# Kernel tuning notes

Measured on AMD Instinct MI355X. Metric: run time of the kernel, lower is better.

Reference implementation:

```python
import math
import jax, jax.numpy as jnp
import numpy as np

B, W, C = 2, 2048, 1024
N, K = 16, 64  # heads, head dim (C // N)


def setup_inputs() -> dict:
    key = jax.random.key(0)
    ks = jax.random.split(key, 6)
    return {
        "in_sequence_bwc": jax.random.normal(ks[0], (B, W, C), dtype=jnp.float32),
        "W_proj": jax.random.normal(ks[1], (C, C), dtype=jnp.float32) * (1.0 / math.sqrt(C)),
        "b_proj": jax.random.normal(ks[2], (C,), dtype=jnp.float32) * 0.01,
        "generators_1nwk": jax.random.normal(ks[3], (1, N, W, K), dtype=jnp.float32),
        "W_mix": jax.random.normal(ks[4], (C, C), dtype=jnp.float32) * (1.0 / math.sqrt(C)),
        "b_mix": jax.random.normal(ks[5], (C,), dtype=jnp.float32) * 0.01,
    }


def reference(in_sequence_bwc, W_proj, b_proj, generators_1nwk, W_mix, b_mix):
    b, w, c = in_sequence_bwc.shape
    # shared projection (torch Linear: x @ W.T + b)
    p_bwc = in_sequence_bwc @ W_proj.T + b_proj
    p_bnwk = p_bwc.reshape(b, w, N, K).transpose(0, 2, 1, 3)  # [b, n, w, k]
    g_nwk = generators_1nwk[0, :, :w, :]  # [n, w, k]
    # data-dependent metric generator: p^T @ G -> [b, n, k, k]
    m_bnkk = jnp.einsum("bnwk,nwl->bnkl", p_bnwk, g_nwk)
    tril_kk = jnp.tril(jnp.ones((K, K), dtype=in_sequence_bwc.dtype))
    m_bnkk = m_bnkk * tril_kk  # lower-triangular mask on k x k
    m_bnkk = m_bnkk @ jnp.swapaxes(m_bnkk, -1, -2)  # PSD metric M M^T
    # bilinear scores: P @ M @ P^T, scaled
    pm_bnwk = jnp.einsum("bnwk,bnkl->bnwl", p_bnwk, m_bnkk)
    scores_bnww = jnp.einsum("bnwk,bnvk->bnwv", pm_bnwk, p_bnwk) / math.sqrt(K)
    causal = jnp.tril(jnp.ones((w, w), dtype=bool))
    scores_bnww = jnp.where(causal, scores_bnww, -jnp.inf)
    attn_bnww = jax.nn.softmax(scores_bnww, axis=-1)
    nudged_bnwk = attn_bnww @ p_bnwk
    nudged_bwc = nudged_bnwk.transpose(0, 2, 1, 3).reshape(b, w, c)
    return nudged_bwc @ W_mix.T + b_mix
```

## Files before the change

### kernel.cpp

```cpp
#include <hip/hip_runtime.h>
#include <math.h>

#define B_  2
#define W_  2048
#define C_  1024
#define NH_ 16
#define KD_ 64

__device__ __forceinline__ int sw(int r, int c) {
    return (r << 6) + ((((c >> 2) ^ ((r >> 2) & 7)) << 2) | (c & 3));
}

__device__ __forceinline__ void stage64s(const float* __restrict__ src,
                                         float* dst, int tid) {
#pragma unroll
    for (int q = 0; q < 4; ++q) {
        int idx = tid + (q << 8);
        int r   = idx >> 4;
        int c   = (idx & 15) << 2;
        *(float4*)&dst[sw(r, c)] = *(const float4*)(src + (idx << 2));
    }
}

__device__ __forceinline__ void stage64(const float* __restrict__ src,
                                        float (*dst)[68], int tid) {
#pragma unroll
    for (int q = 0; q < 4; ++q) {
        int idx = tid + (q << 8);
        int e   = idx << 2;
        int r   = e >> 6;
        int c   = e & 63;
        *(float4*)&dst[r][c] = *(const float4*)(src + e);
    }
}

template<int OUT_P_LAYOUT>
__global__ __launch_bounds__(256, 2)
void gemm_nt(const float* __restrict__ A, const float* __restrict__ Bw,
             const float* __restrict__ bias, float* __restrict__ Cout)
{
    __shared__ float As[16][68];
    __shared__ float Bs[16][68];
    const int tid = threadIdx.x;
    const int tx  = tid & 15, ty = tid >> 4;
    const int m0  = blockIdx.x << 6;
    const int n0  = blockIdx.y << 6;
    const int lrow = tid >> 2;
    const int lkq  = (tid & 3) << 2;
    const float* Ap = A  + (size_t)(m0 + lrow) * C_ + lkq;
    const float* Bp = Bw + (size_t)(n0 + lrow) * C_ + lkq;

    float acc[4][4] = {};
    for (int k0 = 0; k0 < C_; k0 += 16) {
        float4 av = *(const float4*)(Ap + k0);
        float4 bv = *(const float4*)(Bp + k0);
        __syncthreads();
        As[lkq+0][lrow] = av.x; As[lkq+1][lrow] = av.y;
        As[lkq+2][lrow] = av.z; As[lkq+3][lrow] = av.w;
        Bs[lkq+0][lrow] = bv.x; Bs[lkq+1][lrow] = bv.y;
        Bs[lkq+2][lrow] = bv.z; Bs[lkq+3][lrow] = bv.w;
        __syncthreads();
#pragma unroll
        for (int kk = 0; kk < 16; ++kk) {
            float4 a4 = *(const float4*)&As[kk][ty << 2];
            float4 b4 = *(const float4*)&Bs[kk][tx << 2];
            float am[4] = {a4.x, a4.y, a4.z, a4.w};
            float bm[4] = {b4.x, b4.y, b4.z, b4.w};
#pragma unroll
            for (int i = 0; i < 4; ++i)
#pragma unroll
                for (int j = 0; j < 4; ++j)
                    acc[i][j] = fmaf(am[i], bm[j], acc[i][j]);
        }
    }

    const int gc = n0 + (tx << 2);
    float4 bb = *(const float4*)&bias[gc];
#pragma unroll
    for (int i = 0; i < 4; ++i) {
        int gm = m0 + (ty << 2) + i;
        float4 o;
        o.x = acc[i][0] + bb.x;
        o.y = acc[i][1] + bb.y;
        o.z = acc[i][2] + bb.z;
        o.w = acc[i][3] + bb.w;
        if (OUT_P_LAYOUT) {
            int b = gm >> 11;
            int w = gm & 2047;
            int n = gc >> 6;
            int k = gc & 63;
            *(float4*)(Cout + (((size_t)(b * NH_ + n) * W_ + w) * KD_ + k)) = o;
        } else {
            *(float4*)(Cout + (size_t)gm * C_ + gc) = o;
        }
    }
}

__global__ __launch_bounds__(256, 2)
void metric_part(const float* __restrict__ p, const float* __restrict__ g,
                 float* __restrict__ part)
{
    __shared__ float Ps[32][68];
    __shared__ float Gs[32][68];
    const int ch  = blockIdx.x;
    const int bn  = blockIdx.y;
    const int n   = bn & (NH_ - 1);
    const int tid = threadIdx.x;
    const int tx  = tid & 15, ty = tid >> 4;
    const float* pb = p + (size_t)bn * W_ * KD_ + (size_t)(ch << 8) * KD_;
    const float* gb = g + (size_t)n  * W_ * KD_ + (size_t)(ch << 8) * KD_;

    float acc[4][4] = {};
    for (int w0 = 0; w0 < 256; w0 += 32) {
        __syncthreads();
#pragma unroll
        for (int q = 0; q < 2; ++q) {
            int idx = tid + (q << 8);
            int e   = idx << 2;
            int r   = e >> 6;
            int c   = e & 63;
            *(float4*)&Ps[r][c] = *(const float4*)(pb + (size_t)(w0 + r) * KD_ + c);
            *(float4*)&Gs[r][c] = *(const float4*)(gb + (size_t)(w0 + r) * KD_ + c);
        }
        __syncthreads();
#pragma unroll 8
        for (int w = 0; w < 32; ++w) {
            float4 a4 = *(const float4*)&Ps[w][ty << 2];
            float4 b4 = *(const float4*)&Gs[w][tx << 2];
            float am[4] = {a4.x, a4.y, a4.z, a4.w};
            float bm[4] = {b4.x, b4.y, b4.z, b4.w};
#pragma unroll
            for (int i = 0; i < 4; ++i)
#pragma unroll
                for (int j = 0; j < 4; ++j)
                    acc[i][j] = fmaf(am[i], bm[j], acc[i][j]);
        }
    }

    float* ob = part + (size_t)(bn * 8 + ch) * KD_ * KD_;
#pragma unroll
    for (int i = 0; i < 4; ++i) {
        float4 o; o.x = acc[i][0]; o.y = acc[i][1]; o.z = acc[i][2]; o.w = acc[i][3];
        *(float4*)(ob + ((ty << 2) + i) * KD_ + (tx << 2)) = o;
    }
}

__global__ __launch_bounds__(256, 2)
void metric_reduce(const float* __restrict__ part, float* __restrict__ m2)
{
    __shared__ float M1s[64][68];
    const int bn  = blockIdx.x;
    const int tid = threadIdx.x;
    const int tx  = tid & 15, ty = tid >> 4;
    const float* pb = part + (size_t)bn * 8 * KD_ * KD_;

#pragma unroll
    for (int v = 0; v < 4; ++v) {
        int f = tid + (v << 8);
        int e = f << 2;
        float4 s = *(const float4*)(pb + e);
#pragma unroll
        for (int c = 1; c < 8; ++c) {
            float4 t = *(const float4*)(pb + c * 4096 + e);
            s.x += t.x; s.y += t.y; s.z += t.z; s.w += t.w;
        }
        int k = e >> 6, l = e & 63;
        if (l + 0 > k) s.x = 0.f;
        if (l + 1 > k) s.y = 0.f;
        if (l + 2 > k) s.z = 0.f;
        if (l + 3 > k) s.w = 0.f;
        *(float4*)&M1s[k][l] = s;
    }
    __syncthreads();

    float a2[4][4] = {};
#pragma unroll
    for (int jq = 0; jq < 64; jq += 4) {
        float4 av[4], bv[4];
#pragma unroll
        for (int i = 0; i < 4; ++i) av[i] = *(const float4*)&M1s[(ty << 2) + i][jq];
#pragma unroll
        for (int j = 0; j < 4; ++j) bv[j] = *(const float4*)&M1s[(tx << 2) + j][jq];
#pragma unroll
        for (int i = 0; i < 4; ++i)
#pragma unroll
            for (int j = 0; j < 4; ++j)
                a2[i][j] += av[i].x * bv[j].x + av[i].y * bv[j].y +
                            av[i].z * bv[j].z + av[i].w * bv[j].w;
    }

    float* ob = m2 + (size_t)bn * KD_ * KD_;
#pragma unroll
    for (int i = 0; i < 4; ++i) {
        float4 o; o.x = a2[i][0]; o.y = a2[i][1]; o.z = a2[i][2]; o.w = a2[i][3];
        *(float4*)(ob + ((ty << 2) + i) * KD_ + (tx << 2)) = o;
    }
}

__global__ __launch_bounds__(256, 2)
void qgen_k(const float* __restrict__ p, const float* __restrict__ m2,
            float* __restrict__ qout)
{
    __shared__ float Pt[64][68];
    __shared__ float Ms[64][68];
    const int bn  = blockIdx.y;
    const int w0  = blockIdx.x << 6;
    const int tid = threadIdx.x;
    const int tx  = tid & 15, ty = tid >> 4;
    const float* pb = p  + (size_t)bn * W_ * KD_ + (size_t)w0 * KD_;
    const float* mb = m2 + (size_t)bn * KD_ * KD_;

    stage64(pb, Pt, tid);
    stage64(mb, Ms, tid);
    __syncthreads();

    float acc[4][4] = {};
#pragma unroll
    for (int kq = 0; kq < 64; kq += 4) {
        float4 av[4];
        float  bm[4][4];
#pragma unroll
        for (int i = 0; i < 4; ++i) av[i] = *(const float4*)&Pt[(ty << 2) + i][kq];
#pragma unroll
        for (int kk = 0; kk < 4; ++kk) {
            float4 t = *(const float4*)&Ms[kq + kk][tx << 2];
            bm[kk][0] = t.x; bm[kk][1] = t.y; bm[kk][2] = t.z; bm[kk][3] = t.w;
        }
#pragma unroll
        for (int i = 0; i < 4; ++i) {
            float am[4] = {av[i].x, av[i].y, av[i].z, av[i].w};
#pragma unroll
            for (int j = 0; j < 4; ++j)
                acc[i][j] = fmaf(am[0], bm[0][j],
                            fmaf(am[1], bm[1][j],
                            fmaf(am[2], bm[2][j],
                            fmaf(am[3], bm[3][j], acc[i][j]))));
        }
    }

    float* ob = qout + (size_t)bn * W_ * KD_ + (size_t)w0 * KD_;
#pragma unroll
    for (int i = 0; i < 4; ++i) {
        float4 o;
        o.x = acc[i][0] * 0.125f; o.y = acc[i][1] * 0.125f;
        o.z = acc[i][2] * 0.125f; o.w = acc[i][3] * 0.125f;
        *(float4*)(ob + ((ty << 2) + i) * KD_ + (tx << 2)) = o;
    }
}

__global__ __launch_bounds__(256, 2)
void attn_k(const float* __restrict__ qg, const float* __restrict__ p,
            float* __restrict__ nud)
{
    __shared__ float Qs[4096];
    __shared__ float Ks[4096];
    __shared__ float Es[4096];
    const int bid = blockIdx.x;
    const int bn  = bid & 31;
    const int qt  = 31 - (bid >> 5);
    const int b   = bn >> 4, n = bn & 15;
    const int tid = threadIdx.x;
    const int tx  = tid & 15, ty = tid >> 4;
    const float* qb = qg + (size_t)bn * W_ * KD_ + (size_t)(qt << 6) * KD_;
    const float* kb = p  + (size_t)bn * W_ * KD_;

    stage64s(qb, Qs, tid);

    float acc[4][4] = {};
    float mi[4], li[4];
#pragma unroll
    for (int i = 0; i < 4; ++i) { mi[i] = -INFINITY; li[i] = 0.f; }

    for (int j0 = 0; j0 <= qt; ++j0) {
        __syncthreads();
        stage64s(kb + (size_t)(j0 << 6) * KD_, Ks, tid);
        __syncthreads();

        float s[4][4] = {};
#pragma unroll
        for (int kq = 0; kq < 64; kq += 4) {
            float4 av[4], bv[4];
#pragma unroll
            for (int i = 0; i < 4; ++i) av[i] = *(const float4*)&Qs[sw((ty << 2) + i, kq)];
#pragma unroll
            for (int j = 0; j < 4; ++j) bv[j] = *(const float4*)&Ks[sw((tx << 2) + j, kq)];
#pragma unroll
            for (int i = 0; i < 4; ++i)
#pragma unroll
                for (int j = 0; j < 4; ++j)
                    s[i][j] = fmaf(av[i].x, bv[j].x,
                              fmaf(av[i].y, bv[j].y,
                              fmaf(av[i].z, bv[j].z,
                              fmaf(av[i].w, bv[j].w, s[i][j]))));
        }

        if (j0 == qt) {
#pragma unroll
            for (int i = 0; i < 4; ++i)
#pragma unroll
                for (int j = 0; j < 4; ++j)
                    if (((tx << 2) + j) > ((ty << 2) + i)) s[i][j] = -INFINITY;
        }

        float mnew[4], al[4];
#pragma unroll
        for (int i = 0; i < 4; ++i) {
            float rm = fmaxf(fmaxf(s[i][0], s[i][1]), fmaxf(s[i][2], s[i][3]));
            rm = fmaxf(rm, __shfl_xor(rm, 1, 16));
            rm = fmaxf(rm, __shfl_xor(rm, 2, 16));
            rm = fmaxf(rm, __shfl_xor(rm, 4, 16));
            rm = fmaxf(rm, __shfl_xor(rm, 8, 16));
            mnew[i] = fmaxf(mi[i], rm);
        }
#pragma unroll
        for (int i = 0; i < 4; ++i) {
#pragma unroll
            for (int j = 0; j < 4; ++j) s[i][j] = __expf(s[i][j] - mnew[i]);
            float rs = s[i][0] + s[i][1] + s[i][2] + s[i][3];
            rs += __shfl_xor(rs, 1, 16);
            rs += __shfl_xor(rs, 2, 16);
            rs += __shfl_xor(rs, 4, 16);
            rs += __shfl_xor(rs, 8, 16);
            al[i] = __expf(mi[i] - mnew[i]);
            li[i] = li[i] * al[i] + rs;
            mi[i] = mnew[i];
        }
#pragma unroll
        for (int i = 0; i < 4; ++i) {
            float4 e; e.x = s[i][0]; e.y = s[i][1]; e.z = s[i][2]; e.w = s[i][3];
            *(float4*)&Es[sw((ty << 2) + i, tx << 2)] = e;
#pragma unroll
            for (int j = 0; j < 4; ++j) acc[i][j] *= al[i];
        }
        __syncthreads();

#pragma unroll
        for (int jq = 0; jq < 64; jq += 4) {
            float4 av[4];
            float  vm[4][4];
#pragma unroll
            for (int i = 0; i < 4; ++i) av[i] = *(const float4*)&Es[sw((ty << 2) + i, jq)];
#pragma unroll
            for (int kk = 0; kk < 4; ++kk) {
                float4 t = *(const float4*)&Ks[sw(jq + kk, tx << 2)];
                vm[kk][0] = t.x; vm[kk][1] = t.y; vm[kk][2] = t.z; vm[kk][3] = t.w;
            }
#pragma unroll
            for (int i = 0; i < 4; ++i) {
                float am[4] = {av[i].x, av[i].y, av[i].z, av[i].w};
#pragma unroll
                for (int c = 0; c < 4; ++c)
                    acc[i][c] = fmaf(am[0], vm[0][c],
                                fmaf(am[1], vm[1][c],
                                fmaf(am[2], vm[2][c],
                                fmaf(am[3], vm[3][c], acc[i][c]))));
            }
        }
    }

    const int wrow = qt << 6;
#pragma unroll
    for (int i = 0; i < 4; ++i) {
        float inv = 1.f / li[i];
        float4 o;
        o.x = acc[i][0] * inv; o.y = acc[i][1] * inv;
        o.z = acc[i][2] * inv; o.w = acc[i][3] * inv;
        size_t row = (size_t)(b * W_ + wrow + (ty << 2) + i);
        *(float4*)(nud + row * C_ + (n << 6) + (tx << 2)) = o;
    }
}

extern "C" void kernel_launch(void* const* d_in, const int* in_sizes, int n_in,
                              void* d_out, int out_size, void* d_ws, size_t ws_size,
                              hipStream_t stream)
{
    (void)in_sizes; (void)n_in; (void)out_size; (void)ws_size;
    const float* X  = (const float*)d_in[0];
    const float* Wp = (const float*)d_in[1];
    const float* bp = (const float*)d_in[2];
    const float* G  = (const float*)d_in[3];
    const float* Wm = (const float*)d_in[4];
    const float* bm = (const float*)d_in[5];
    float* out = (float*)d_out;
    float* ws  = (float*)d_ws;

    float* Pbuf = ws;
    float* Qbuf = ws + 4194304;
    float* M2   = ws + 8388608;
    float* Nud  = ws + 8519680;
    float* Part = Qbuf;

    dim3 blk(256);
    gemm_nt<1>   <<<dim3(64, 16), blk, 0, stream>>>(X, Wp, bp, Pbuf);
    metric_part  <<<dim3(8, 32),  blk, 0, stream>>>(Pbuf, G, Part);
    metric_reduce<<<dim3(32),     blk, 0, stream>>>(Part, M2);
    qgen_k       <<<dim3(32, 32), blk, 0, stream>>>(Pbuf, M2, Qbuf);
    attn_k       <<<dim3(1024),   blk, 0, stream>>>(Qbuf, Pbuf, Nud);
    gemm_nt<0>   <<<dim3(64, 16), blk, 0, stream>>>(Nud, Wm, bm, out);
}
```

Before: 855.5 us.

## Read Q and K tiles directly from global memory in attention kernel

Removes the shared-memory staging of the Q and K/V tiles in the attention kernel and loads them straight from global memory (relying on L1/L2 caching), keeping only the probability tile in LDS. This drops two barriers per key tile and cuts LDS use, which allows raising the launch-bounds occupancy target from 2 to 4 blocks per CU. The block-to-query-tile mapping is also changed so blocks past the first 512 walk query tiles in ascending order. The risk is many redundant, poorly coalesced global loads, since each thread reads rows strided by 64 floats and the tiles are re-read per thread group instead of once per block.

```diff
diff --git a/kernel.cpp b/kernel.cpp
--- a/kernel.cpp
+++ b/kernel.cpp
@@ -9,17 +9,6 @@
 
 __device__ __forceinline__ int sw(int r, int c) {
     return (r << 6) + ((((c >> 2) ^ ((r >> 2) & 7)) << 2) | (c & 3));
-}
-
-__device__ __forceinline__ void stage64s(const float* __restrict__ src,
-                                         float* dst, int tid) {
-#pragma unroll
-    for (int q = 0; q < 4; ++q) {
-        int idx = tid + (q << 8);
-        int r   = idx >> 4;
-        int c   = (idx & 15) << 2;
-        *(float4*)&dst[sw(r, c)] = *(const float4*)(src + (idx << 2));
-    }
 }
 
 __device__ __forceinline__ void stage64(const float* __restrict__ src,
@@ -248,42 +237,41 @@
     }
 }
 
-__global__ __launch_bounds__(256, 2)
+__global__ __launch_bounds__(256, 4)
 void attn_k(const float* __restrict__ qg, const float* __restrict__ p,
             float* __restrict__ nud)
 {
-    __shared__ float Qs[4096];
-    __shared__ float Ks[4096];
     __shared__ float Es[4096];
     const int bid = blockIdx.x;
     const int bn  = bid & 31;
-    const int qt  = 31 - (bid >> 5);
+    const int qt  = (bid < 512) ? (31 - (bid >> 5)) : ((bid - 512) >> 5);
     const int b   = bn >> 4, n = bn & 15;
     const int tid = threadIdx.x;
     const int tx  = tid & 15, ty = tid >> 4;
     const float* qb = qg + (size_t)bn * W_ * KD_ + (size_t)(qt << 6) * KD_;
     const float* kb = p  + (size_t)bn * W_ * KD_;
 
-    stage64s(qb, Qs, tid);
-
     float acc[4][4] = {};
     float mi[4], li[4];
 #pragma unroll
     for (int i = 0; i < 4; ++i) { mi[i] = -INFINITY; li[i] = 0.f; }
 
+    const float* qv = qb;
+
     for (int j0 = 0; j0 <= qt; ++j0) {
-        __syncthreads();
-        stage64s(kb + (size_t)(j0 << 6) * KD_, Ks, tid);
-        __syncthreads();
+        asm volatile("" : "+v"(qv));
+        const float* kt = kb + (size_t)(j0 << 6) * KD_;
 
         float s[4][4] = {};
 #pragma unroll
-        for (int kq = 0; kq < 64; kq += 4) {
+        for (int kq = 0; kq < 16; ++kq) {
             float4 av[4], bv[4];
 #pragma unroll
-            for (int i = 0; i < 4; ++i) av[i] = *(const float4*)&Qs[sw((ty << 2) + i, kq)];
-#pragma unroll
-            for (int j = 0; j < 4; ++j) bv[j] = *(const float4*)&Ks[sw((tx << 2) + j, kq)];
+            for (int i = 0; i < 4; ++i)
+                av[i] = *(const float4*)(qv + ((ty << 2) + i) * KD_ + (kq << 2));
+#pragma unroll
+            for (int j = 0; j < 4; ++j)
+                bv[j] = *(const float4*)(kt + ((tx << 2) + j) * KD_ + (kq << 2));
 #pragma unroll
             for (int i = 0; i < 4; ++i)
 #pragma unroll
@@ -325,6 +313,8 @@
             li[i] = li[i] * al[i] + rs;
             mi[i] = mnew[i];
         }
+
+        __syncthreads();
 #pragma unroll
         for (int i = 0; i < 4; ++i) {
             float4 e; e.x = s[i][0]; e.y = s[i][1]; e.z = s[i][2]; e.w = s[i][3];
@@ -342,7 +332,7 @@
             for (int i = 0; i < 4; ++i) av[i] = *(const float4*)&Es[sw((ty << 2) + i, jq)];
 #pragma unroll
             for (int kk = 0; kk < 4; ++kk) {
-                float4 t = *(const float4*)&Ks[sw(jq + kk, tx << 2)];
+                float4 t = *(const float4*)(kt + (size_t)(jq + kk) * KD_ + (tx << 2));
                 vm[kk][0] = t.x; vm[kk][1] = t.y; vm[kk][2] = t.z; vm[kk][3] = t.w;
             }
 #pragma unroll
```

New measurement: 1.069 ms. 1.25x slower.

## Double-buffer K tiles with register prefetch in attention kernel

Applied to the files above, without the earlier changes.

The attention kernel now keeps two shared-memory K buffers. It loads the next K tile into registers while computing scores for the current one, then writes it to the alternate buffer before the PV pass. This overlaps global-load latency with compute and removes one barrier per iteration. It also reorders block-to-query-tile assignment so the second half of blocks walks light tiles in ascending order, at the cost of more LDS and register pressure.

```diff
diff --git a/kernel.cpp b/kernel.cpp
--- a/kernel.cpp
+++ b/kernel.cpp
@@ -253,11 +253,11 @@
             float* __restrict__ nud)
 {
     __shared__ float Qs[4096];
-    __shared__ float Ks[4096];
+    __shared__ float Ks[2][4096];
     __shared__ float Es[4096];
     const int bid = blockIdx.x;
     const int bn  = bid & 31;
-    const int qt  = 31 - (bid >> 5);
+    const int qt  = (bid < 512) ? (31 - (bid >> 5)) : ((bid - 512) >> 5);
     const int b   = bn >> 4, n = bn & 15;
     const int tid = threadIdx.x;
     const int tx  = tid & 15, ty = tid >> 4;
@@ -265,25 +265,37 @@
     const float* kb = p  + (size_t)bn * W_ * KD_;
 
     stage64s(qb, Qs, tid);
+    stage64s(kb, Ks[0], tid);
+    __syncthreads();
 
     float acc[4][4] = {};
     float mi[4], li[4];
 #pragma unroll
     for (int i = 0; i < 4; ++i) { mi[i] = -INFINITY; li[i] = 0.f; }
 
+    float4 ld[4];
+
     for (int j0 = 0; j0 <= qt; ++j0) {
-        __syncthreads();
-        stage64s(kb + (size_t)(j0 << 6) * KD_, Ks, tid);
-        __syncthreads();
+        const int cur = j0 & 1;
+        float* Kc = Ks[cur];
+
+        if (j0 < qt) {
+            const float* nx = kb + (size_t)((j0 + 1) << 6) * KD_;
+#pragma unroll
+            for (int q = 0; q < 4; ++q)
+                ld[q] = *(const float4*)(nx + ((tid + (q << 8)) << 2));
+        }
 
         float s[4][4] = {};
 #pragma unroll
-        for (int kq = 0; kq < 64; kq += 4) {
+        for (int kq = 0; kq < 16; ++kq) {
             float4 av[4], bv[4];
 #pragma unroll
-            for (int i = 0; i < 4; ++i) av[i] = *(const float4*)&Qs[sw((ty << 2) + i, kq)];
-#pragma unroll
-            for (int j = 0; j < 4; ++j) bv[j] = *(const float4*)&Ks[sw((tx << 2) + j, kq)];
+            for (int i = 0; i < 4; ++i)
+                av[i] = *(const float4*)&Qs[sw((ty << 2) + i, kq << 2)];
+#pragma unroll
+            for (int j = 0; j < 4; ++j)
+                bv[j] = *(const float4*)&Kc[sw((tx << 2) + j, kq << 2)];
 #pragma unroll
             for (int i = 0; i < 4; ++i)
 #pragma unroll
@@ -325,6 +337,9 @@
             li[i] = li[i] * al[i] + rs;
             mi[i] = mnew[i];
         }
+
+        __syncthreads();
+
 #pragma unroll
         for (int i = 0; i < 4; ++i) {
             float4 e; e.x = s[i][0]; e.y = s[i][1]; e.z = s[i][2]; e.w = s[i][3];
@@ -332,6 +347,14 @@
 #pragma unroll
             for (int j = 0; j < 4; ++j) acc[i][j] *= al[i];
         }
+        if (j0 < qt) {
+            float* Kn = Ks[cur ^ 1];
+#pragma unroll
+            for (int q = 0; q < 4; ++q) {
+                int idx = tid + (q << 8);
+                *(float4*)&Kn[sw(idx >> 4, (idx & 15) << 2)] = ld[q];
+            }
+        }
         __syncthreads();
 
 #pragma unroll
@@ -342,7 +365,7 @@
             for (int i = 0; i < 4; ++i) av[i] = *(const float4*)&Es[sw((ty << 2) + i, jq)];
 #pragma unroll
             for (int kk = 0; kk < 4; ++kk) {
-                float4 t = *(const float4*)&Ks[sw(jq + kk, tx << 2)];
+                float4 t = *(const float4*)&Kc[sw(jq + kk, tx << 2)];
                 vm[kk][0] = t.x; vm[kk][1] = t.y; vm[kk][2] = t.z; vm[kk][3] = t.w;
             }
 #pragma unroll
```

After: 802.6 us. -6.2%, faster.
